# Optimization experiments

Measured on AMD Instinct MI355X. Metric: run time of the kernel, lower is better.

The kernel has to match this reference:

```python
import jax, jax.numpy as jnp
import numpy as np


def setup_inputs() -> dict:
    key = jax.random.key(0)
    k1, k2, k3, k4, k5 = jax.random.split(key, 5)
    B, S, E, H, D = 8, 1024, 1024, 8, 128  # batch, seq, embed, heads, hidden/head
    stdv = 1.0 / np.sqrt(D)
    return {
        "k": jax.random.normal(k1, (B, S, E), jnp.float32),
        "q": jax.random.normal(k2, (B, S, E), jnp.float32),
        "flag": 0,  # False: project q through w_qx
        "w_kx": jax.random.uniform(k3, (H, E, D), jnp.float32, -stdv, stdv),
        "w_qx": jax.random.uniform(k4, (H, E, D), jnp.float32, -stdv, stdv),
        "proj_w": jax.random.normal(k5, (E, H * D), jnp.float32) * 0.02,  # out_dim = embed_dim
        "proj_b": jnp.zeros((E,), jnp.float32),
    }


def reference(k, q, flag, w_kx, w_qx, proj_w, proj_b):
    H, E, D = w_kx.shape
    B, Sk, _ = k.shape
    Sq = q.shape[1]
    # per-head tanh projections: [H, B, S, D]
    kx = jnp.tanh(jnp.einsum("bse,hed->hbsd", k, w_kx))
    if flag:
        qx = jnp.broadcast_to(q[None], (H,) + q.shape)  # q already in hidden space
    else:
        qx = jnp.tanh(jnp.einsum("bse,hed->hbsd", q, w_qx))
    # scaled dot product scores [H, B, Sq, Sk]
    score = jnp.einsum("hbqd,hbkd->hbqk", qx, kx) / jnp.sqrt(jnp.float32(D))
    attn = jax.nn.softmax(score, axis=-1)
    out = jnp.einsum("hbqk,hbkd->hbqd", attn, kx)  # [H, B, Sq, D]
    # concat heads: [B, Sq, H*D], then output projection (dropout p=0 is identity)
    out = jnp.transpose(out, (1, 2, 0, 3)).reshape(B, Sq, H * D)
    return out @ proj_w.T + proj_b
```

## Files before the change

kernel.cpp:

```cpp
#include <hip/hip_runtime.h>

typedef unsigned short u16;
typedef unsigned int u32;
typedef __bf16 bf16x8 __attribute__((ext_vector_type(8)));
typedef float f32x4 __attribute__((ext_vector_type(4)));

#define MFMA16(a, b, c) __builtin_amdgcn_mfma_f32_16x16x32_bf16(a, b, c, 0, 0, 0)
#define EXP2(x) __builtin_amdgcn_exp2f(x)

typedef const void __attribute__((address_space(1)))* gas1_t;
typedef void __attribute__((address_space(3)))* las3_t;

__device__ __forceinline__ void gload16(const void* g, void* l) {
  __builtin_amdgcn_global_load_lds((gas1_t)g, (las3_t)l, 16, 0, 0);
}

__device__ __forceinline__ u16 f2bf(float f) {
  union { float f; u32 u; } v; v.f = f;
  u32 r = v.u + 0x7FFFu + ((v.u >> 16) & 1u);
  return (u16)(r >> 16);
}

__device__ __forceinline__ float fast_tanh(float x) {
  float xc = fminf(fmaxf(x, -20.f), 20.f);
  float t = EXP2(xc * 2.885390081777927f);
  return (t - 1.0f) * __builtin_amdgcn_rcpf(t + 1.0f);
}

__global__ __launch_bounds__(256) void cvt_kernel(const float* __restrict__ in,
                                                  u16* __restrict__ out, int n8) {
  int i = blockIdx.x * blockDim.x + threadIdx.x;
  int stride = gridDim.x * blockDim.x;
  for (; i < n8; i += stride) {
    const float4* p = (const float4*)(in + (size_t)i * 8);
    float4 a = p[0], b = p[1];
    u16 t[8];
    t[0] = f2bf(a.x); t[1] = f2bf(a.y); t[2] = f2bf(a.z); t[3] = f2bf(a.w);
    t[4] = f2bf(b.x); t[5] = f2bf(b.y); t[6] = f2bf(b.z); t[7] = f2bf(b.w);
    *(uint4*)(out + (size_t)i * 8) = *(uint4*)t;
  }
}

__global__ __launch_bounds__(256) void wtrans_kernel(const float* __restrict__ w,
                                                     u16* __restrict__ wT) {
  __shared__ float t[64][65];
  int h = blockIdx.z;
  int e0 = blockIdx.x * 64, d0 = blockIdx.y * 64;
  const float* src = w + (size_t)h * 1024 * 128;
  u16* dst = wT + (size_t)h * 128 * 1024;
  int tid = threadIdx.x;
  {
    int row = tid >> 2, c0 = (tid & 3) * 16;
#pragma unroll
    for (int i = 0; i < 4; ++i) {
      float4 v = *(const float4*)(src + (size_t)(e0 + row) * 128 + d0 + c0 + i * 4);
      t[row][c0 + i * 4 + 0] = v.x;
      t[row][c0 + i * 4 + 1] = v.y;
      t[row][c0 + i * 4 + 2] = v.z;
      t[row][c0 + i * 4 + 3] = v.w;
    }
  }
  __syncthreads();
  {
    int dl = tid >> 2, c0 = (tid & 3) * 16;
    u16 tmp[16];
#pragma unroll
    for (int i = 0; i < 16; ++i) tmp[i] = f2bf(t[c0 + i][dl]);
    u16* o = dst + (size_t)(d0 + dl) * 1024 + e0 + c0;
    *(uint4*)o = *(uint4*)tmp;
    *(uint4*)(o + 8) = *(uint4*)(tmp + 8);
  }
}

template <int AR, int BR, int WM, int WN>
__device__ __forceinline__ void gemm_core_big(const u16* __restrict__ Abase,
                                              const u16* __restrict__ Bbase,
                                              int K, u16* lds,
                                              f32x4 (&acc)[AR / (WM * 16)][BR / (WN * 16)]) {
  constexpr int MF = AR / (WM * 16), NFR = BR / (WN * 16);
  constexpr int NA = AR / 64, NB = BR / 64;
  constexpr int AL = AR * 64, BL = BR * 64;
  const int tid = threadIdx.x, lane = tid & 63, wid = tid >> 6;
  const int wr = wid / WN, wc = wid % WN;
  const int l15 = lane & 15, g = lane >> 4;
  u16* A0 = lds;
  u16* B0 = lds + AL;
  u16* A1 = lds + AL + BL;
  u16* B1 = lds + 2 * AL + BL;
  const int nkt = K >> 6;

#define STGX(dst, srcb, NI, kt_)                                                \
  _Pragma("unroll") for (int i_ = 0; i_ < (NI); ++i_) {                         \
    int c = (wid * (NI) + i_) * 64 + lane;                                      \
    int row = c >> 3, slot = c & 7, src = slot ^ (row & 7);                     \
    gload16((const char*)(srcb) + ((size_t)row * K + (kt_) * 64 + src * 8) * 2, \
            (char*)(dst) + (wid * (NI) + i_) * 1024);                           \
  }

#define VWAIT()                                                                 \
  do {                                                                          \
    if constexpr (NA + NB == 8) asm volatile("s_waitcnt vmcnt(8)" ::: "memory");\
    else                        asm volatile("s_waitcnt vmcnt(6)" ::: "memory");\
  } while (0)

#define CMPX(Al, Bl)                                                            \
  do {                                                                          \
    __builtin_amdgcn_s_setprio(1);                                              \
    _Pragma("unroll") for (int kc = 0; kc < 2; ++kc) {                          \
      bf16x8 af[MF], bb[NFR];                                                   \
      _Pragma("unroll") for (int f = 0; f < MF; ++f) {                          \
        int rp = wr * (AR / WM) + f * 16 + l15;                                 \
        af[f] = *(const bf16x8*)((Al) + rp * 64 + (((kc * 4 + g) ^ (rp & 7)) << 3)); \
      }                                                                         \
      _Pragma("unroll") for (int f = 0; f < NFR; ++f) {                         \
        int rp = wc * (BR / WN) + f * 16 + l15;                                 \
        bb[f] = *(const bf16x8*)((Bl) + rp * 64 + (((kc * 4 + g) ^ (rp & 7)) << 3)); \
      }                                                                         \
      _Pragma("unroll") for (int mf = 0; mf < MF; ++mf)                         \
        _Pragma("unroll") for (int nf = 0; nf < NFR; ++nf)                      \
          acc[mf][nf] = MFMA16(af[mf], bb[nf], acc[mf][nf]);                    \
    }                                                                           \
    __builtin_amdgcn_s_setprio(0);                                              \
  } while (0)

  STGX(A0, Abase, NA, 0);
  STGX(B0, Bbase, NB, 0);
  for (int it = 0; it < nkt / 2 - 1; ++it) {
    STGX(A1, Abase, NA, 2 * it + 1);
    STGX(B1, Bbase, NB, 2 * it + 1);
    VWAIT();
    __builtin_amdgcn_s_barrier();
    CMPX(A0, B0);
    __builtin_amdgcn_s_barrier();
    STGX(A0, Abase, NA, 2 * it + 2);
    STGX(B0, Bbase, NB, 2 * it + 2);
    VWAIT();
    __builtin_amdgcn_s_barrier();
    CMPX(A1, B1);
    __builtin_amdgcn_s_barrier();
  }
  STGX(A1, Abase, NA, nkt - 1);
  STGX(B1, Bbase, NB, nkt - 1);
  VWAIT();
  __builtin_amdgcn_s_barrier();
  CMPX(A0, B0);
  asm volatile("s_waitcnt vmcnt(0)" ::: "memory");
  __builtin_amdgcn_s_barrier();
  CMPX(A1, B1);
#undef STGX
#undef VWAIT
#undef CMPX
}

__global__ __launch_bounds__(512, 2) void gemm_tanh_kernel(
    const u16* __restrict__ Ak, const u16* __restrict__ Aq,
    const u16* __restrict__ wTk, const u16* __restrict__ wTq,
    u16* __restrict__ kxo, u16* __restrict__ qxo) {
  __shared__ alignas(16) u16 lds[2 * (256 * 64 + 256 * 64)];
  const u16* A; const u16* W; u16* C;
  if (blockIdx.z == 0) { A = Ak; W = wTk; C = kxo; }
  else { A = Aq; W = wTq; C = qxo; }
  int mBase = blockIdx.x * 256;
  int nBase = blockIdx.y * 256;
  f32x4 acc[8][4];
#pragma unroll
  for (int i = 0; i < 8; ++i)
#pragma unroll
    for (int j = 0; j < 4; ++j) acc[i][j] = (f32x4){0.f, 0.f, 0.f, 0.f};
  gemm_core_big<256, 256, 2, 4>(A + (size_t)mBase * 1024,
                                W + (size_t)nBase * 1024, 1024, lds, acc);
  const int lane = threadIdx.x & 63, wid = threadIdx.x >> 6;
  const int wr = wid >> 2, wc = wid & 3, l15 = lane & 15, g = lane >> 4;
#pragma unroll
  for (int mf = 0; mf < 8; ++mf)
#pragma unroll
    for (int nf = 0; nf < 4; ++nf)
#pragma unroll
      for (int j = 0; j < 4; ++j) {
        int m = mBase + wr * 128 + mf * 16 + g * 4 + j;
        int n = nBase + wc * 64 + nf * 16 + l15;
        int h = n >> 7, d = n & 127;
        C[(size_t)h * 8192 * 128 + (size_t)m * 128 + d] =
            f2bf(fast_tanh(acc[mf][nf][j]));
      }
}

__global__ __launch_bounds__(256) void transpose_kernel(const u16* __restrict__ kx,
                                                        u16* __restrict__ kxT) {
  __shared__ u16 t[64][72];
  int hb = blockIdx.z;
  const u16* src = kx + (size_t)hb * 1024 * 128;
  u16* dst = kxT + (size_t)hb * 128 * 1024;
  int s0 = blockIdx.x * 64, d0 = blockIdx.y * 64;
  int tid = threadIdx.x;
#pragma unroll
  for (int r = 0; r < 2; ++r) {
    int row = r * 32 + (tid >> 3), c8 = (tid & 7) * 8;
    uint4 v = *(const uint4*)(src + (size_t)(s0 + row) * 128 + d0 + c8);
    *(uint4*)&t[row][c8] = v;
  }
  __syncthreads();
#pragma unroll
  for (int r = 0; r < 2; ++r) {
    int dl = r * 32 + (tid >> 3), s8 = (tid & 7) * 8;
    u16 tmp[8];
#pragma unroll
    for (int i = 0; i < 8; ++i) tmp[i] = t[s8 + i][dl];
    *(uint4*)(dst + (size_t)(d0 + dl) * 1024 + s0 + s8) = *(uint4*)tmp;
  }
}

__global__ __launch_bounds__(256, 2) void attn_kernel(const u16* __restrict__ qx,
                                                      const u16* __restrict__ kx,
                                                      const u16* __restrict__ kxT,
                                                      u16* __restrict__ X) {
  __shared__ alignas(16) u16 Klds[2][64 * 128];
  __shared__ alignas(16) u16 Vlds[2][128 * 64];
  __shared__ alignas(16) u16 Plds[4][32 * 64];
  const int tid = threadIdx.x, lane = tid & 63, wid = tid >> 6;
  const int g = lane >> 4;
  const int hb = blockIdx.x, qt = blockIdx.y, h = hb >> 3, b = hb & 7;
  const u16* qxh = qx + ((size_t)h * 8192 + (size_t)b * 1024) * 128;
  const u16* kxh = kx + ((size_t)h * 8192 + (size_t)b * 1024) * 128;
  const u16* kxTh = kxT + (size_t)hb * 128 * 1024;
  const int q0 = qt * 128 + wid * 32;
  const float SC = 0.08838834764831845f * 1.44269504088896340f;

#define STAGE(buf, kt_)                                                        \
  do {                                                                         \
    _Pragma("unroll") for (int i_ = 0; i_ < 4; ++i_) {                         \
      int cIdx = (wid * 4 + i_) * 64 + lane;                                   \
      {                                                                        \
        int row = cIdx >> 4, slot = cIdx & 15;                                 \
        int src = slot ^ (row & 7);                                            \
        gload16((const char*)kxh + (size_t)((kt_) * 64 + row) * 256 + src * 16,\
                (char*)&Klds[buf][0] + (wid * 4 + i_) * 1024);                 \
      }                                                                        \
      {                                                                        \
        int row = cIdx >> 3, slot = cIdx & 7;                                  \
        int src = slot ^ (row & 7);                                            \
        gload16((const char*)kxTh + (size_t)row * 2048 + (kt_) * 128 + src * 16,\
                (char*)&Vlds[buf][0] + (wid * 4 + i_) * 1024);                 \
      }                                                                        \
    }                                                                          \
  } while (0)

  bf16x8 qa[2][4];
#pragma unroll
  for (int m = 0; m < 2; ++m)
#pragma unroll
    for (int kc = 0; kc < 4; ++kc)
      qa[m][kc] = *(const bf16x8*)(qxh + (size_t)(q0 + m * 16 + (lane & 15)) * 128
                                   + kc * 32 + g * 8);

  f32x4 os[2][8];
#pragma unroll
  for (int i = 0; i < 2; ++i)
#pragma unroll
    for (int j = 0; j < 8; ++j) os[i][j] = (f32x4){0.f, 0.f, 0.f, 0.f};
  float lsum[2] = {0.f, 0.f};

  u16* Pw = &Plds[wid][0];

  STAGE(0, 0);

  for (int kt = 0; kt < 16; ++kt) {
    const int cur = kt & 1;
    if (kt < 15) {
      STAGE(cur ^ 1, kt + 1);
      asm volatile("s_waitcnt vmcnt(8)" ::: "memory");
    } else {
      asm volatile("s_waitcnt vmcnt(0)" ::: "memory");
    }
    __builtin_amdgcn_s_barrier();

    const u16* Kc = &Klds[cur][0];
    const u16* Vc = &Vlds[cur][0];

    f32x4 sa[4][2];
#pragma unroll
    for (int i = 0; i < 4; ++i)
#pragma unroll
      for (int j = 0; j < 2; ++j) sa[i][j] = (f32x4){0.f, 0.f, 0.f, 0.f};
    __builtin_amdgcn_s_setprio(1);
#pragma unroll
    for (int kc = 0; kc < 4; ++kc) {
      bf16x8 kb[4];
#pragma unroll
      for (int t = 0; t < 4; ++t) {
        int row = t * 16 + (lane & 15);
        int ch = kc * 4 + g;
        kb[t] = *(const bf16x8*)(Kc + row * 128 + ((ch ^ (row & 7)) << 3));
      }
#pragma unroll
      for (int t = 0; t < 4; ++t)
#pragma unroll
        for (int m = 0; m < 2; ++m)
          sa[t][m] = MFMA16(kb[t], qa[m][kc], sa[t][m]);
    }
    __builtin_amdgcn_s_setprio(0);

#pragma unroll
    for (int m = 0; m < 2; ++m) {
      int q = m * 16 + (lane & 15);
      int rowb = q * 128, q7 = q & 7;
#pragma unroll
      for (int t = 0; t < 4; ++t) {
        float p0 = EXP2(sa[t][m][0] * SC);
        float p1 = EXP2(sa[t][m][1] * SC);
        float p2 = EXP2(sa[t][m][2] * SC);
        float p3 = EXP2(sa[t][m][3] * SC);
        lsum[m] += (p0 + p1) + (p2 + p3);
        uint2 pk;
        pk.x = (u32)f2bf(p0) | ((u32)f2bf(p1) << 16);
        pk.y = (u32)f2bf(p2) | ((u32)f2bf(p3) << 16);
        int slot = (2 * t + (g >> 1)) ^ q7;
        *(uint2*)((char*)Pw + rowb + slot * 16 + 8 * (g & 1)) = pk;
      }
    }

    __builtin_amdgcn_s_setprio(1);
#pragma unroll
    for (int kc2 = 0; kc2 < 2; ++kc2) {
      bf16x8 pa[2], vb[8];
#pragma unroll
      for (int m = 0; m < 2; ++m) {
        int q = m * 16 + (lane & 15);
        int slot = (g + 4 * kc2) ^ (q & 7);
        pa[m] = *(const bf16x8*)((char*)Pw + q * 128 + slot * 16);
      }
#pragma unroll
      for (int nd = 0; nd < 8; ++nd) {
        int row = nd * 16 + (lane & 15);
        int ch = kc2 * 4 + g;
        vb[nd] = *(const bf16x8*)(Vc + row * 64 + ((ch ^ (row & 7)) << 3));
      }
#pragma unroll
      for (int m = 0; m < 2; ++m)
#pragma unroll
        for (int nd = 0; nd < 8; ++nd)
          os[m][nd] = MFMA16(pa[m], vb[nd], os[m][nd]);
    }
    __builtin_amdgcn_s_setprio(0);
    __builtin_amdgcn_s_barrier();
  }
#undef STAGE

#pragma unroll
  for (int m = 0; m < 2; ++m) {
    float s = lsum[m];
    s += __shfl_xor(s, 16);
    s += __shfl_xor(s, 32);
    lsum[m] = s;
  }

#pragma unroll
  for (int m = 0; m < 2; ++m)
#pragma unroll
    for (int j = 0; j < 4; ++j) {
      float tot = __shfl(lsum[m], 4 * g + j, 64);
      float inv = 1.f / tot;
      int qrow = b * 1024 + q0 + m * 16 + g * 4 + j;
#pragma unroll
      for (int nd = 0; nd < 8; ++nd) {
        int col = h * 128 + nd * 16 + (lane & 15);
        X[(size_t)qrow * 1024 + col] = f2bf(os[m][nd][j] * inv);
      }
    }
}

__global__ __launch_bounds__(512, 2) void gemm_bias_kernel(
    const u16* __restrict__ X, const u16* __restrict__ pw,
    const float* __restrict__ pb, float* __restrict__ out) {
  __shared__ alignas(16) u16 lds[2 * (256 * 64 + 128 * 64)];
  int mBase = blockIdx.x * 256;
  int nBase = blockIdx.y * 128;
  f32x4 acc[4][4];
#pragma unroll
  for (int i = 0; i < 4; ++i)
#pragma unroll
    for (int j = 0; j < 4; ++j) acc[i][j] = (f32x4){0.f, 0.f, 0.f, 0.f};
  gemm_core_big<256, 128, 4, 2>(X + (size_t)mBase * 1024,
                                pw + (size_t)nBase * 1024, 1024, lds, acc);
  const int lane = threadIdx.x & 63, wid = threadIdx.x >> 6;
  const int wr = wid >> 1, wc = wid & 1, l15 = lane & 15, g = lane >> 4;
#pragma unroll
  for (int nf = 0; nf < 4; ++nf) {
    int e = nBase + wc * 64 + nf * 16 + l15;
    float bv = pb[e];
#pragma unroll
    for (int mf = 0; mf < 4; ++mf)
#pragma unroll
      for (int j = 0; j < 4; ++j) {
        int m = mBase + wr * 64 + mf * 16 + g * 4 + j;
        out[(size_t)m * 1024 + e] = acc[mf][nf][j] + bv;
      }
  }
}

extern "C" void kernel_launch(void* const* d_in, const int* in_sizes, int n_in,
                              void* d_out, int out_size, void* d_ws, size_t ws_size,
                              hipStream_t stream) {
  const float* k = (const float*)d_in[0];
  const float* q = (const float*)d_in[1];
  const float* wk = (const float*)d_in[3];
  const float* wq = (const float*)d_in[4];
  const float* pw = (const float*)d_in[5];
  const float* pb = (const float*)d_in[6];
  float* out = (float*)d_out;
  char* ws = (char*)d_ws;

  u16* kbf = (u16*)(ws);
  u16* qbf = (u16*)(ws + (16ull << 20));
  u16* wTk = (u16*)(ws + (32ull << 20));
  u16* wTq = (u16*)(ws + (34ull << 20));
  u16* pwb = (u16*)(ws + (36ull << 20));
  u16* kx  = (u16*)(ws + (38ull << 20));
  u16* qx  = (u16*)(ws + (54ull << 20));
  u16* kxT = (u16*)(ws + (70ull << 20));
  u16* X   = kbf;

  cvt_kernel<<<2048, 256, 0, stream>>>(k, kbf, 1048576);
  cvt_kernel<<<2048, 256, 0, stream>>>(q, qbf, 1048576);
  cvt_kernel<<<512, 256, 0, stream>>>(pw, pwb, 131072);
  wtrans_kernel<<<dim3(16, 2, 8), 256, 0, stream>>>(wk, wTk);
  wtrans_kernel<<<dim3(16, 2, 8), 256, 0, stream>>>(wq, wTq);
  gemm_tanh_kernel<<<dim3(32, 4, 2), 512, 0, stream>>>(kbf, qbf, wTk, wTq, kx, qx);
  transpose_kernel<<<dim3(16, 2, 64), 256, 0, stream>>>(kx, kxT);
  attn_kernel<<<dim3(64, 8), 256, 0, stream>>>(qx, kx, kxT, X);
  gemm_bias_kernel<<<dim3(32, 8), 512, 0, stream>>>(X, pwb, pb, out);
}
```

Measured before the change: 137.4 us.

## Restructure GEMM core into finer-grained half-tile staging with interleaved prefetch

Replaces the double-buffered GEMM core with a version that stages each 64-wide K tile as two 32-wide halves. Each half's A and B prefetch is issued between MFMA sub-phases, splitting each K step into four barrier-separated compute phases. The aim is to overlap global-to-LDS loads more finely with matrix math and shrink the LDS footprint. The output-projection GEMM retiles from 256x128 to 128x256 blocks with an 8-wave 2x4 layout. This adds more barriers per K step and uses a new swizzle, which risks extra sync overhead or LDS bank conflicts.

```diff
diff --git a/kernel.cpp b/kernel.cpp
--- a/kernel.cpp
+++ b/kernel.cpp
@@ -72,91 +72,127 @@
   }
 }
 
-template <int AR, int BR, int WM, int WN>
-__device__ __forceinline__ void gemm_core_big(const u16* __restrict__ Abase,
-                                              const u16* __restrict__ Bbase,
-                                              int K, u16* lds,
-                                              f32x4 (&acc)[AR / (WM * 16)][BR / (WN * 16)]) {
-  constexpr int MF = AR / (WM * 16), NFR = BR / (WN * 16);
-  constexpr int NA = AR / 64, NB = BR / 64;
-  constexpr int AL = AR * 64, BL = BR * 64;
+
+template <int NI>
+__device__ __forceinline__ void stageT(u16* dst, const u16* src, int K, int koff,
+                                       int wid, int lane) {
+#pragma unroll
+  for (int i = 0; i < NI; ++i) {
+    int c = (wid * NI + i) * 64 + lane;
+    int lr = c >> 3, dsl = c & 7;
+    int ssl = dsl ^ (lr & 7);
+    int grow = lr * 2 + (ssl >> 2);
+    int gk = koff + (ssl & 3) * 8;
+    gload16((const char*)src + ((size_t)grow * K + gk) * 2, (char*)dst + c * 16);
+  }
+}
+
+__device__ __forceinline__ bf16x8 ldfrag(const u16* half, int rp, int g) {
+  int lr = rp >> 1;
+  int slot = (((rp & 1) << 2) | g) ^ (lr & 7);
+  return *(const bf16x8*)(half + lr * 64 + slot * 8);
+}
+
+template <int BM>
+__device__ __forceinline__ void gemm8_core(const u16* __restrict__ Ab,
+                                           const u16* __restrict__ Bb,
+                                           int K, u16* lds,
+                                           f32x4 (&acc)[BM / 32][4]) {
+  constexpr int MF = BM / 32, MH = MF / 2;
+  constexpr int AH = (BM / 2) * 64;
+  constexpr int BH = 128 * 64;
+  constexpr int BUF = 2 * AH + 2 * BH;
+  constexpr int NIA = BM / 128;
   const int tid = threadIdx.x, lane = tid & 63, wid = tid >> 6;
-  const int wr = wid / WN, wc = wid % WN;
-  const int l15 = lane & 15, g = lane >> 4;
-  u16* A0 = lds;
-  u16* B0 = lds + AL;
-  u16* A1 = lds + AL + BL;
-  u16* B1 = lds + 2 * AL + BL;
+  const int wr = wid >> 2, wc = wid & 3, l15 = lane & 15, g = lane >> 4;
   const int nkt = K >> 6;
-
-#define STGX(dst, srcb, NI, kt_)                                                \
-  _Pragma("unroll") for (int i_ = 0; i_ < (NI); ++i_) {                         \
-    int c = (wid * (NI) + i_) * 64 + lane;                                      \
-    int row = c >> 3, slot = c & 7, src = slot ^ (row & 7);                     \
-    gload16((const char*)(srcb) + ((size_t)row * K + (kt_) * 64 + src * 8) * 2, \
-            (char*)(dst) + (wid * (NI) + i_) * 1024);                           \
-  }
-
-#define VWAIT()                                                                 \
+  const int arow0 = wr * (BM / 2);
+
+#define VWAITN()                                                                \
   do {                                                                          \
-    if constexpr (NA + NB == 8) asm volatile("s_waitcnt vmcnt(8)" ::: "memory");\
-    else                        asm volatile("s_waitcnt vmcnt(6)" ::: "memory");\
+    if constexpr (NIA == 2) asm volatile("s_waitcnt vmcnt(4)" ::: "memory");    \
+    else                    asm volatile("s_waitcnt vmcnt(3)" ::: "memory");    \
   } while (0)
 
-#define CMPX(Al, Bl)                                                            \
-  do {                                                                          \
-    __builtin_amdgcn_s_setprio(1);                                              \
-    _Pragma("unroll") for (int kc = 0; kc < 2; ++kc) {                          \
-      bf16x8 af[MF], bb[NFR];                                                   \
-      _Pragma("unroll") for (int f = 0; f < MF; ++f) {                          \
-        int rp = wr * (AR / WM) + f * 16 + l15;                                 \
-        af[f] = *(const bf16x8*)((Al) + rp * 64 + (((kc * 4 + g) ^ (rp & 7)) << 3)); \
-      }                                                                         \
-      _Pragma("unroll") for (int f = 0; f < NFR; ++f) {                         \
-        int rp = wc * (BR / WN) + f * 16 + l15;                                 \
-        bb[f] = *(const bf16x8*)((Bl) + rp * 64 + (((kc * 4 + g) ^ (rp & 7)) << 3)); \
-      }                                                                         \
-      _Pragma("unroll") for (int mf = 0; mf < MF; ++mf)                         \
-        _Pragma("unroll") for (int nf = 0; nf < NFR; ++nf)                      \
-          acc[mf][nf] = MFMA16(af[mf], bb[nf], acc[mf][nf]);                    \
-    }                                                                           \
-    __builtin_amdgcn_s_setprio(0);                                              \
-  } while (0)
-
-  STGX(A0, Abase, NA, 0);
-  STGX(B0, Bbase, NB, 0);
-  for (int it = 0; it < nkt / 2 - 1; ++it) {
-    STGX(A1, Abase, NA, 2 * it + 1);
-    STGX(B1, Bbase, NB, 2 * it + 1);
-    VWAIT();
-    __builtin_amdgcn_s_barrier();
-    CMPX(A0, B0);
-    __builtin_amdgcn_s_barrier();
-    STGX(A0, Abase, NA, 2 * it + 2);
-    STGX(B0, Bbase, NB, 2 * it + 2);
-    VWAIT();
-    __builtin_amdgcn_s_barrier();
-    CMPX(A1, B1);
-    __builtin_amdgcn_s_barrier();
-  }
-  STGX(A1, Abase, NA, nkt - 1);
-  STGX(B1, Bbase, NB, nkt - 1);
-  VWAIT();
-  __builtin_amdgcn_s_barrier();
-  CMPX(A0, B0);
-  asm volatile("s_waitcnt vmcnt(0)" ::: "memory");
-  __builtin_amdgcn_s_barrier();
-  CMPX(A1, B1);
-#undef STGX
-#undef VWAIT
-#undef CMPX
+  stageT<NIA>(lds, Ab, K, 0, wid, lane);
+  stageT<2>(lds + 2 * AH, Bb, K, 0, wid, lane);
+  stageT<NIA>(lds + AH, Ab, K, 32, wid, lane);
+  stageT<2>(lds + 2 * AH + BH, Bb, K, 32, wid, lane);
+
+  for (int t = 0; t < nkt; ++t) {
+    const int cur = t & 1;
+    u16* Ac = lds + cur * BUF;
+    u16* Bc = Ac + 2 * AH;
+    u16* An = lds + (cur ^ 1) * BUF;
+    u16* Bn = An + 2 * AH;
+    const bool pf = (t + 1 < nkt);
+    const int k1 = (t + 1) * 64;
+    bf16x8 af[MH], bb[4];
+
+    VWAITN();
+    __builtin_amdgcn_s_barrier();
+    if (pf) stageT<NIA>(An, Ab, K, k1, wid, lane);
+#pragma unroll
+    for (int m = 0; m < MH; ++m) af[m] = ldfrag(Ac, arow0 + m * 16 + l15, g);
+#pragma unroll
+    for (int n = 0; n < 4; ++n) bb[n] = ldfrag(Bc, wc * 64 + n * 16 + l15, g);
+    __builtin_amdgcn_s_setprio(1);
+#pragma unroll
+    for (int m = 0; m < MH; ++m)
+#pragma unroll
+      for (int n = 0; n < 4; ++n) acc[m][n] = MFMA16(af[m], bb[n], acc[m][n]);
+    __builtin_amdgcn_s_setprio(0);
+
+    __builtin_amdgcn_s_barrier();
+    if (pf) stageT<2>(Bn, Bb, K, k1, wid, lane);
+#pragma unroll
+    for (int m = 0; m < MH; ++m)
+      af[m] = ldfrag(Ac, arow0 + (MH + m) * 16 + l15, g);
+    __builtin_amdgcn_s_setprio(1);
+#pragma unroll
+    for (int m = 0; m < MH; ++m)
+#pragma unroll
+      for (int n = 0; n < 4; ++n)
+        acc[MH + m][n] = MFMA16(af[m], bb[n], acc[MH + m][n]);
+    __builtin_amdgcn_s_setprio(0);
+
+    if (pf) VWAITN();
+    else asm volatile("s_waitcnt vmcnt(0)" ::: "memory");
+    __builtin_amdgcn_s_barrier();
+    if (pf) stageT<NIA>(An + AH, Ab, K, k1 + 32, wid, lane);
+#pragma unroll
+    for (int m = 0; m < MH; ++m) af[m] = ldfrag(Ac + AH, arow0 + m * 16 + l15, g);
+#pragma unroll
+    for (int n = 0; n < 4; ++n) bb[n] = ldfrag(Bc + BH, wc * 64 + n * 16 + l15, g);
+    __builtin_amdgcn_s_setprio(1);
+#pragma unroll
+    for (int m = 0; m < MH; ++m)
+#pragma unroll
+      for (int n = 0; n < 4; ++n) acc[m][n] = MFMA16(af[m], bb[n], acc[m][n]);
+    __builtin_amdgcn_s_setprio(0);
+
+    __builtin_amdgcn_s_barrier();
+    if (pf) stageT<2>(Bn + BH, Bb, K, k1 + 32, wid, lane);
+#pragma unroll
+    for (int m = 0; m < MH; ++m)
+      af[m] = ldfrag(Ac + AH, arow0 + (MH + m) * 16 + l15, g);
+    __builtin_amdgcn_s_setprio(1);
+#pragma unroll
+    for (int m = 0; m < MH; ++m)
+#pragma unroll
+      for (int n = 0; n < 4; ++n)
+        acc[MH + m][n] = MFMA16(af[m], bb[n], acc[MH + m][n]);
+    __builtin_amdgcn_s_setprio(0);
+    __builtin_amdgcn_s_barrier();
+  }
+#undef VWAITN
 }
 
 __global__ __launch_bounds__(512, 2) void gemm_tanh_kernel(
     const u16* __restrict__ Ak, const u16* __restrict__ Aq,
     const u16* __restrict__ wTk, const u16* __restrict__ wTq,
     u16* __restrict__ kxo, u16* __restrict__ qxo) {
-  __shared__ alignas(16) u16 lds[2 * (256 * 64 + 256 * 64)];
+  __shared__ alignas(16) u16 lds[2 * (2 * 128 * 64 + 2 * 128 * 64)];
   const u16* A; const u16* W; u16* C;
   if (blockIdx.z == 0) { A = Ak; W = wTk; C = kxo; }
   else { A = Aq; W = wTq; C = qxo; }
@@ -167,8 +203,8 @@
   for (int i = 0; i < 8; ++i)
 #pragma unroll
     for (int j = 0; j < 4; ++j) acc[i][j] = (f32x4){0.f, 0.f, 0.f, 0.f};
-  gemm_core_big<256, 256, 2, 4>(A + (size_t)mBase * 1024,
-                                W + (size_t)nBase * 1024, 1024, lds, acc);
+  gemm8_core<256>(A + (size_t)mBase * 1024, W + (size_t)nBase * 1024, 1024,
+                  lds, acc);
   const int lane = threadIdx.x & 63, wid = threadIdx.x >> 6;
   const int wr = wid >> 2, wc = wid & 3, l15 = lane & 15, g = lane >> 4;
 #pragma unroll
@@ -372,18 +408,18 @@
 __global__ __launch_bounds__(512, 2) void gemm_bias_kernel(
     const u16* __restrict__ X, const u16* __restrict__ pw,
     const float* __restrict__ pb, float* __restrict__ out) {
-  __shared__ alignas(16) u16 lds[2 * (256 * 64 + 128 * 64)];
-  int mBase = blockIdx.x * 256;
-  int nBase = blockIdx.y * 128;
+  __shared__ alignas(16) u16 lds[2 * (2 * 64 * 64 + 2 * 128 * 64)];
+  int mBase = blockIdx.x * 128;
+  int nBase = blockIdx.y * 256;
   f32x4 acc[4][4];
 #pragma unroll
   for (int i = 0; i < 4; ++i)
 #pragma unroll
     for (int j = 0; j < 4; ++j) acc[i][j] = (f32x4){0.f, 0.f, 0.f, 0.f};
-  gemm_core_big<256, 128, 4, 2>(X + (size_t)mBase * 1024,
-                                pw + (size_t)nBase * 1024, 1024, lds, acc);
+  gemm8_core<128>(X + (size_t)mBase * 1024, pw + (size_t)nBase * 1024, 1024,
+                  lds, acc);
   const int lane = threadIdx.x & 63, wid = threadIdx.x >> 6;
-  const int wr = wid >> 1, wc = wid & 1, l15 = lane & 15, g = lane >> 4;
+  const int wr = wid >> 2, wc = wid & 3, l15 = lane & 15, g = lane >> 4;
 #pragma unroll
   for (int nf = 0; nf < 4; ++nf) {
     int e = nBase + wc * 64 + nf * 16 + l15;
@@ -428,5 +464,5 @@
   gemm_tanh_kernel<<<dim3(32, 4, 2), 512, 0, stream>>>(kbf, qbf, wTk, wTq, kx, qx);
   transpose_kernel<<<dim3(16, 2, 64), 256, 0, stream>>>(kx, kxT);
   attn_kernel<<<dim3(64, 8), 256, 0, stream>>>(qx, kx, kxT, X);
-  gemm_bias_kernel<<<dim3(32, 8), 512, 0, stream>>>(X, pwb, pb, out);
-}
+  gemm_bias_kernel<<<dim3(64, 4), 512, 0, stream>>>(X, pwb, pb, out);
+}
```

Result: no change. 138.2 us (+0.6%).
